# Kernel tuning notes

Measured on AMD Instinct MI355X. Metric: run time of the kernel, lower is better.

## Reference

```python
import jax, jax.numpy as jnp
import numpy as np

EPS = 1e-5  # BatchNorm eps (torch default)


def _norm_adj(adj):
    # DenseGCNConv: add self-loops, symmetric degree normalization
    N = adj.shape[-1]
    adj = adj + jnp.eye(N, dtype=adj.dtype)
    d = jnp.clip(adj.sum(-1), 1.0, None) ** -0.5
    return d[..., :, None] * adj * d[..., None, :]


def _gcn(x, adj_norm, W, b):
    return jnp.einsum('bij,bjf->bif', adj_norm, x @ W) + b


def _batchnorm(h, gamma, beta):
    # torch BatchNorm1d in training mode over flattened (B*N, C)
    B, N, C = h.shape
    hf = h.reshape(B * N, C)
    mu = hf.mean(0)
    var = hf.var(0)  # biased, as used for normalization
    out = (hf - mu) * jax.lax.rsqrt(var + EPS) * gamma + beta
    return out.reshape(B, N, C)


def setup_inputs() -> dict:
    key = jax.random.key(0)
    ks = jax.random.split(key, 24)
    B, N, F, H, D = 4, 256, 6, 128, 256
    s = 0.05
    a = jax.random.uniform(ks[1], (B, N, N), dtype=jnp.float32)
    adj = ((a + jnp.swapaxes(a, 1, 2)) / 2 < 0.1).astype(jnp.float32)  # sparse symmetric adjacency
    return {
        'x': jax.random.normal(ks[0], (B, N, F), dtype=jnp.float32),
        'adj': adj,
        'W1': jax.random.normal(ks[2], (F, H)) * s, 'b1': jnp.zeros((H,)),
        'W2': jax.random.normal(ks[3], (H, H)) * s, 'b2': jnp.zeros((H,)),
        'W3': jax.random.normal(ks[4], (H, D)) * s, 'b3': jnp.zeros((D,)),
        'g1': jnp.ones((H,)), 'beta1': jnp.zeros((H,)),
        'g2': jnp.ones((H,)), 'beta2': jnp.zeros((H,)),
        'e1w': jax.random.normal(ks[5], (2 * D, H)) * s, 'e1b': jnp.zeros((H,)),
        'e2w': jax.random.normal(ks[6], (H, H // 2)) * s, 'e2b': jnp.zeros((H // 2,)),
        'e3w': jax.random.normal(ks[7], (H // 2, 1)) * s, 'e3b': jnp.zeros((1,)),
        'f1w': jax.random.normal(ks[8], (D, H)) * s, 'f1b': jnp.zeros((H,)),
        'f2w': jax.random.normal(ks[9], (H, H)) * s, 'f2b': jnp.zeros((H,)),
        'f3w': jax.random.normal(ks[10], (H, F)) * s, 'f3b': jnp.zeros((F,)),
    }


def reference(x, adj, W1, b1, W2, b2, W3, b3, g1, beta1, g2, beta2,
              e1w, e1b, e2w, e2b, e3w, e3b, f1w, f1b, f2w, f2b, f3w, f3b):
    adj_norm = _norm_adj(adj)
    h = jax.nn.relu(_batchnorm(_gcn(x, adj_norm, W1, b1), g1, beta1))
    h = jax.nn.relu(_batchnorm(_gcn(h, adj_norm, W2, b2), g2, beta2))
    h = jax.nn.relu(_gcn(h, adj_norm, W3, b3))  # [B,N,D]
    D = h.shape[-1]
    # AdjacencyDecoder: Linear(cat(h_i,h_j)) == h_i@e1w[:D] + h_j@e1w[D:] (fused form, same math)
    hi = h @ e1w[:D]   # [B,N,H]
    hj = h @ e1w[D:]   # [B,N,H]
    p = jax.nn.relu(hi[:, :, None, :] + hj[:, None, :, :] + e1b)  # [B,N,N,H]
    p = jax.nn.relu(p @ e2w + e2b)                                 # [B,N,N,H/2]
    logits = (p @ e3w + e3b)[..., 0]                               # [B,N,N]
    logits = (logits + jnp.swapaxes(logits, 1, 2)) / 2
    adj_pred = jax.nn.sigmoid(logits)
    # FeatureDecoder
    f = jax.nn.relu(h @ f1w + f1b)
    f = jax.nn.relu(f @ f2w + f2b)
    feat_pred = f @ f3w + f3b
    return adj_pred, feat_pred
```

## Files before the change

kernel.cpp:

```cpp
#include <hip/hip_runtime.h>


typedef float v4f __attribute__((ext_vector_type(4)));
typedef short v8s __attribute__((ext_vector_type(8)));

__device__ __forceinline__ unsigned short f2bs(float f) {
    union { float f; unsigned int u; } v;
    v.f = f;
    return (unsigned short)((v.u + 0x7fffu + ((v.u >> 16) & 1u)) >> 16);
}

__global__ void k_pre(const float* x, const float* W1, const float* adj,
                      const float* e2w, float* buf, float* dg,
                      unsigned short* bfr_g, float* st) {
    __shared__ float ss[256];
    int blk = blockIdx.x, tid = threadIdx.x;
    if (blk < 512) {
        int idx = blk * 256 + tid;
        int m = idx >> 7, n = idx & 127;
        float s = 0.f;
        for (int k = 0; k < 6; k++) s += x[m * 6 + k] * W1[k * 128 + n];
        buf[idx] = s;
    } else if (blk < 768) {
        int row = (blk - 512) * 4 + (tid >> 6);
        int lane = tid & 63;
        const float* ap = adj + (long)row * 256;
        ss[tid] = ap[lane] + ap[lane + 64] + ap[lane + 128] + ap[lane + 192];
        __syncthreads();
        for (int o = 32; o > 0; o >>= 1) {
            if (lane < o) ss[tid] += ss[tid + o];
            __syncthreads();
        }
        if (lane == 0) {
            float t = ss[tid] + 1.f;
            if (t < 1.f) t = 1.f;
            dg[row] = rsqrtf(t);
        }
    } else {
        for (int s = tid; s < 8192; s += 256) {
            int k = s >> 6, n = s & 63;
            int kc = k >> 5, q = (k & 31) >> 3, t = k & 7;
            int nt = n >> 4, c2 = n & 15;
            bfr_g[(((nt * 4 + kc) * 64) + q * 16 + c2) * 8 + t] = f2bs(e2w[s]);
        }
        st[tid] = 0.f;
        st[256 + tid] = 0.f;
    }
}

template <int K>
__device__ __forceinline__ void dev_tile(
        int t, const float* A, const float* B, const float* bias,
        const float* dgA, float* anOut,
        const float* stat, const float* g, const float* beta,
        float* ostat, float* C,
        int N, int relu,
        int sA, int sB, int sC, int tiles_n, int tiles_m,
        float* smem) {
    constexpr int strideA = K + 4;
    constexpr int NCH = K / 16;
    float* As = smem;
    float* Bs = smem + 4160;
    int tid = threadIdx.x;
    int n2 = tid & 15, ml = tid >> 4;
    int bx = t % tiles_n;
    int tmp = t / tiles_n;
    int by = tmp % tiles_m;
    int bz = tmp / tiles_m;
    int m0 = by * 16, n0 = bx * 32;
    const float* Ab = A + (long)bz * sA;
    const float* Bb = B + (long)bz * sB;
    float* Cb = C + (long)bz * sC;
    const float* dgb = (dgA != 0) ? (dgA + bz * 256) : 0;

    int kk = tid & 15, mm = tid >> 4;
    int nb = tid & 31, kb = tid >> 5;

    float b0_r[NCH], b1_r[NCH], a_r[NCH];
    const float* Arow = Ab + (long)(m0 + mm) * K;
    #pragma unroll
    for (int i = 0; i < NCH; i++) {
        a_r[i]  = Arow[i * 16 + kk];
        b0_r[i] = Bb[(long)(i * 16 + kb) * N + n0 + nb];
        b1_r[i] = Bb[(long)(i * 16 + kb + 8) * N + n0 + nb];
    }

    if (dgA != 0) {
        float di = dgb[m0 + mm];
        float d_r[NCH];
        #pragma unroll
        for (int i = 0; i < NCH; i++) d_r[i] = dgb[i * 16 + kk];
        #pragma unroll
        for (int i = 0; i < NCH; i++) {
            int kg = i * 16 + kk;
            float v = a_r[i];
            if (m0 + mm == kg) v += 1.f;
            v = di * v * d_r[i];
            if (anOut != 0 && bx == 0)
                anOut[bz * 65536 + (m0 + mm) * 256 + kg] = v;
            As[mm * strideA + kg] = v;
        }
    } else if (stat != 0) {
        float s_r[NCH], q_r[NCH], g_r[NCH], be_r[NCH];
        #pragma unroll
        for (int i = 0; i < NCH; i++) {
            int kg = i * 16 + kk;
            s_r[i]  = stat[kg];
            q_r[i]  = stat[128 + kg];
            g_r[i]  = g[kg];
            be_r[i] = beta[kg];
        }
        #pragma unroll
        for (int i = 0; i < NCH; i++) {
            int kg = i * 16 + kk;
            float mu = s_r[i] * (1.f / 1024.f);
            float vr = q_r[i] * (1.f / 1024.f) - mu * mu;
            float sc = rsqrtf(vr + 1e-5f) * g_r[i];
            float v = (a_r[i] - mu) * sc + be_r[i];
            if (v < 0.f) v = 0.f;
            As[mm * strideA + kg] = v;
        }
    } else {
        #pragma unroll
        for (int i = 0; i < NCH; i++)
            As[mm * strideA + i * 16 + kk] = a_r[i];
    }
    #pragma unroll
    for (int i = 0; i < NCH; i++) {
        Bs[(i * 16 + kb) * 32 + nb] = b0_r[i];
        Bs[(i * 16 + kb + 8) * 32 + nb] = b1_r[i];
    }
    __syncthreads();

    float c0a = 0.f, c0b = 0.f, c1a = 0.f, c1b = 0.f;
    const float* arow = As + ml * strideA;
    const float* bcol = Bs + n2 * 2;
    #pragma unroll
    for (int q0 = 0; q0 < K; q0 += 4) {
        float4 av = *(const float4*)(arow + q0);
        float2 b0 = *(const float2*)(bcol + (q0 + 0) * 32);
        float2 b1 = *(const float2*)(bcol + (q0 + 1) * 32);
        float2 b2 = *(const float2*)(bcol + (q0 + 2) * 32);
        float2 b3 = *(const float2*)(bcol + (q0 + 3) * 32);
        c0a += av.x * b0.x; c1a += av.x * b0.y;
        c0b += av.y * b1.x; c1b += av.y * b1.y;
        c0a += av.z * b2.x; c1a += av.z * b2.y;
        c0b += av.w * b3.x; c1b += av.w * b3.y;
    }
    float c0 = c0a + c0b, c1 = c1a + c1b;
    int mRow = m0 + ml, nn = n0 + n2 * 2;
    if (bias != 0) { c0 += bias[nn]; c1 += bias[nn + 1]; }
    if (relu) {
        if (c0 < 0.f) c0 = 0.f;
        if (c1 < 0.f) c1 = 0.f;
    }
    Cb[(long)mRow * N + nn] = c0;
    Cb[(long)mRow * N + nn + 1] = c1;

    if (ostat != 0) {
        float* sred = smem;
        float* qred = smem + 544;
        __syncthreads();
        sred[(n2 * 2) * 17 + ml] = c0;
        sred[(n2 * 2 + 1) * 17 + ml] = c1;
        qred[(n2 * 2) * 17 + ml] = c0 * c0;
        qred[(n2 * 2 + 1) * 17 + ml] = c1 * c1;
        __syncthreads();
        if (tid < 32) {
            float s = 0.f, q = 0.f;
            for (int u = 0; u < 16; u++) {
                s += sred[tid * 17 + u];
                q += qred[tid * 17 + u];
            }
            atomicAdd(&ostat[n0 + tid], s);
            atomicAdd(&ostat[128 + n0 + tid], q);
        }
    }
}

template <int K>
__global__ __launch_bounds__(256, 3) void k_tgemm(
        const float* A, const float* B, const float* bias,
        const float* dgA, float* anOut,
        const float* stat, const float* g, const float* beta,
        float* ostat, float* C,
        int N, int relu,
        int sA, int sB, int sC, int tiles_n, int tiles_m) {
    __shared__ float smem[12352];
    dev_tile<K>(blockIdx.x, A, B, bias, dgA, anOut, stat, g, beta, ostat, C,
                N, relu, sA, sB, sC, tiles_n, tiles_m, smem);
}

__global__ __launch_bounds__(256, 3) void k_g67(
        const float* hb, const float* e1w, float* hi,
        const float* f1w, const float* f1b, float* f1) {
    __shared__ float smem[12352];
    int t = blockIdx.x;
    if (t < 512) {
        dev_tile<256>(t, hb, e1w, 0, 0, 0, 0, 0, 0, 0, hi,
                      128, 0, 0, 32768, 131072, 4, 64, smem);
    } else {
        dev_tile<256>(t - 512, hb, f1w, f1b, 0, 0, 0, 0, 0, 0, f1,
                      128, 1, 0, 0, 0, 4, 64, smem);
    }
}

__global__ void k_decf(const float* hi, const float* hj, const float* e1b,
                       const unsigned short* bfr_g, const float* e2b,
                       const float* e3w, const float* e3b,
                       const float* f1, const float* f2w, const float* f2b_,
                       const float* f3w, const float* f3b,
                       float* lg, float* out) {
    __shared__ float smem[4608];
    int tid = threadIdx.x;
    int blk = blockIdx.x;
    if (blk < 1024) {
        float* red = smem;
        float* pre_sh = smem + 4352;
        int lane = tid & 63, wv = tid >> 6;
        int col = lane & 15, quad = lane >> 4;
        int bi = blk, b = bi >> 8;
        if (tid < 128) pre_sh[tid] = hi[bi * 128 + tid] + e1b[tid];
        __syncthreads();
        float e2bv[4], e3wv[4];
        for (int nt = 0; nt < 4; nt++) {
            e2bv[nt] = e2b[nt * 16 + col];
            e3wv[nt] = e3w[nt * 16 + col];
        }
        const float* hjb = hj + b * 32768;
        #pragma unroll 1
        for (int ms = 0; ms < 4; ms++) {
            v4f acc[4];
            for (int nt = 0; nt < 4; nt++) {
                v4f z = {0.f, 0.f, 0.f, 0.f};
                acc[nt] = z;
            }
            int j = wv * 64 + ms * 16 + col;
            const float* rowp = hjb + j * 128 + quad * 8;
            float hjr[32];
            #pragma unroll
            for (int q = 0; q < 8; q++) {
                float4 v = *(const float4*)(rowp + (q >> 1) * 32 + (q & 1) * 4);
                hjr[q * 4 + 0] = v.x; hjr[q * 4 + 1] = v.y;
                hjr[q * 4 + 2] = v.z; hjr[q * 4 + 3] = v.w;
            }
            #pragma unroll
            for (int kc = 0; kc < 4; kc++) {
                const float* pp = pre_sh + kc * 32 + quad * 8;
                v8s af;
                #pragma unroll
                for (int t = 0; t < 8; t++) {
                    float p = pp[t] + hjr[kc * 8 + t];
                    p = (p > 0.f) ? p : 0.f;
                    af[t] = (short)f2bs(p);
                }
                #pragma unroll
                for (int nt = 0; nt < 4; nt++) {
                    v8s bf = *(const v8s*)&bfr_g[(((nt * 4 + kc) * 64) + lane) * 8];
                    acc[nt] = __builtin_amdgcn_mfma_f32_16x16x32_bf16(
                        af, bf, acc[nt], 0, 0, 0);
                }
            }
            #pragma unroll
            for (int r = 0; r < 4; r++) {
                float s = 0.f;
                #pragma unroll
                for (int nt = 0; nt < 4; nt++) {
                    float v = acc[nt][r] + e2bv[nt];
                    if (v > 0.f) s += v * e3wv[nt];
                }
                red[(wv * 64 + ms * 16 + quad * 4 + r) * 17 + col] = s;
            }
        }
        __syncthreads();
        float s = e3b[0];
        for (int c = 0; c < 16; c++) s += red[tid * 17 + c];
        lg[bi * 256 + tid] = s;
    } else {
        float* f2row = smem;
        int r0 = (blk - 1024) * 4;
        for (int p = 0; p < 2; p++) {
            int idx = tid + p * 256;
            int r = r0 + (idx >> 7), n = idx & 127;
            const float* f1r = f1 + (long)r * 128;
            float s0 = 0.f, s1 = 0.f, s2 = 0.f, s3 = 0.f;
            #pragma unroll
            for (int k = 0; k < 128; k += 4) {
                float4 fv = *(const float4*)(f1r + k);
                s0 += fv.x * f2w[(k + 0) * 128 + n];
                s1 += fv.y * f2w[(k + 1) * 128 + n];
                s2 += fv.z * f2w[(k + 2) * 128 + n];
                s3 += fv.w * f2w[(k + 3) * 128 + n];
            }
            float s = f2b_[n] + ((s0 + s1) + (s2 + s3));
            if (s < 0.f) s = 0.f;
            f2row[idx] = s;
        }
        __syncthreads();
        if (tid < 24) {
            int r = tid / 6, c = tid % 6;
            float s = f3b[c];
            const float* fr = f2row + r * 128;
            for (int k = 0; k < 128; k++) s += fr[k] * f3w[k * 6 + c];
            out[262144 + (r0 + r) * 6 + c] = s;
        }
    }
}

__global__ void k_symsig(const float* lg, float* out) {
    __shared__ float Ta[32 * 33];
    __shared__ float Tb[32 * 33];
    int tid = threadIdx.x;
    int b = blockIdx.x / 36;
    int t = blockIdx.x % 36;
    int ti = 0, rem = t;
    while (rem >= 8 - ti) { rem -= 8 - ti; ti++; }
    int tj = ti + rem;
    int i0 = ti * 32, j0 = tj * 32;
    const float* lgb = lg + b * 65536;
    for (int p = 0; p < 4; p++) {
        int idx = p * 256 + tid;
        int r = idx >> 5, c = idx & 31;
        Ta[r * 33 + c] = lgb[(i0 + r) * 256 + j0 + c];
        Tb[r * 33 + c] = lgb[(j0 + r) * 256 + i0 + c];
    }
    __syncthreads();
    float* ob = out + b * 65536;
    for (int p = 0; p < 4; p++) {
        int idx = p * 256 + tid;
        int r = idx >> 5, c = idx & 31;
        float v1 = 0.5f * (Ta[r * 33 + c] + Tb[c * 33 + r]);
        ob[(i0 + r) * 256 + j0 + c] = 1.f / (1.f + expf(-v1));
        float v2 = 0.5f * (Tb[r * 33 + c] + Ta[c * 33 + r]);
        ob[(j0 + r) * 256 + i0 + c] = 1.f / (1.f + expf(-v2));
    }
}

extern "C" void kernel_launch(void* const* d_in, const int* in_sizes, int n_in,
                              void* d_out, int out_size, void* d_ws, size_t ws_size,
                              hipStream_t stream) {
    const float* x   = (const float*)d_in[0];
    const float* adj = (const float*)d_in[1];
    const float* W1  = (const float*)d_in[2];
    const float* b1  = (const float*)d_in[3];
    const float* W2  = (const float*)d_in[4];
    const float* b2  = (const float*)d_in[5];
    const float* W3  = (const float*)d_in[6];
    const float* b3  = (const float*)d_in[7];
    const float* g1  = (const float*)d_in[8];
    const float* be1 = (const float*)d_in[9];
    const float* g2  = (const float*)d_in[10];
    const float* be2 = (const float*)d_in[11];
    const float* e1w = (const float*)d_in[12];
    const float* e1b = (const float*)d_in[13];
    const float* e2w = (const float*)d_in[14];
    const float* e2b = (const float*)d_in[15];
    const float* e3w = (const float*)d_in[16];
    const float* e3b = (const float*)d_in[17];
    const float* f1w = (const float*)d_in[18];
    const float* f1b = (const float*)d_in[19];
    const float* f2w = (const float*)d_in[20];
    const float* f2b_ = (const float*)d_in[21];
    const float* f3w = (const float*)d_in[22];
    const float* f3b = (const float*)d_in[23];

    float* out = (float*)d_out;

    if (ws_size < (size_t)1600000 * 4) {
        hipMemsetAsync(d_out, 0x60, 4096, stream);
        return;
    }
    float* ws = (float*)d_ws;
    float* st1 = ws;
    float* st2 = ws + 256;
    float* dg  = ws + 512;
    unsigned short* bfr_g = (unsigned short*)(ws + 1536);
    float* An  = ws + 5632;
    float* buf = An + 262144;
    float* hb  = buf + 262144;
    float* lg  = hb + 262144;
    float* h1  = lg + 262144;
    float* h2  = h1 + 131072;
    float* hi  = h2 + 131072;
    float* hj  = hi + 131072;

    k_pre<<<769, 256, 0, stream>>>(x, W1, adj, e2w, buf, dg, bfr_g, st1);
    k_tgemm<256><<<256, 256, 0, stream>>>(adj, buf, b1, dg, An, 0, 0, 0, st1, h1,
                                          128, 0, 65536, 32768, 32768, 4, 16);
    k_tgemm<128><<<256, 256, 0, stream>>>(h1, W2, 0, 0, 0, st1, g1, be1, 0, buf,
                                          128, 0, 0, 0, 0, 4, 64);
    k_tgemm<256><<<256, 256, 0, stream>>>(An, buf, b2, 0, 0, 0, 0, 0, st2, h2,
                                          128, 0, 65536, 32768, 32768, 4, 16);
    k_tgemm<128><<<512, 256, 0, stream>>>(h2, W3, 0, 0, 0, st2, g2, be2, 0, buf,
                                          256, 0, 0, 0, 0, 8, 64);
    k_tgemm<256><<<512, 256, 0, stream>>>(An, buf, b3, 0, 0, 0, 0, 0, 0, hb,
                                          256, 1, 65536, 65536, 65536, 8, 16);
    k_g67<<<768, 256, 0, stream>>>(hb, e1w, hi, f1w, f1b, h1);
    k_decf<<<1280, 256, 0, stream>>>(hi, hj, e1b, bfr_g, e2b, e3w, e3b,
                                     h1, f2w, f2b_, f3w, f3b, lg, out);
    k_symsig<<<144, 256, 0, stream>>>(lg, out);
}
```

Before: 184.3 us.

## Fuse BN+ReLU, adjacency aggregation and weight GEMM into one kernel per GCN layer

```diff
diff --git a/kernel.cpp b/kernel.cpp
--- a/kernel.cpp
+++ b/kernel.cpp
@@ -189,6 +189,117 @@
     __shared__ float smem[12352];
     dev_tile<K>(blockIdx.x, A, B, bias, dgA, anOut, stat, g, beta, ostat, C,
                 N, relu, sA, sB, sC, tiles_n, tiles_m, smem);
+}
+
+template <int NW, int NC, int STATS, int RELU>
+__global__ __launch_bounds__(512, 1) void k_fuse2(
+        const float* __restrict__ An, const float* __restrict__ Hin,
+        const float* __restrict__ W, const float* __restrict__ bias,
+        const float* __restrict__ st, const float* __restrict__ g,
+        const float* __restrict__ beta, float* ostat, float* OUT) {
+    __shared__ float sm[15360];
+    float* sl  = sm;
+    float* sh  = sm + 128;
+    float* An_s = sm + 256;
+    float* P_s  = sm + 4416;
+    float* Ws   = sm + 8640;
+    float* T_s  = sm + 13248;
+
+    int t = threadIdx.x;
+    int bx = blockIdx.x;
+    int nc = bx % NC;
+    int mt = (bx / NC) & 15;
+    int bz = bx / (NC * 16);
+    int m0 = mt * 16;
+    int r = t >> 5, cg = t & 31;
+
+    const float* Ag = An + (long)bz * 65536 + (long)(m0 + r) * 256 + cg * 8;
+    float4 anA = *(const float4*)Ag;
+    float4 anB = *(const float4*)(Ag + 4);
+    const float* Hg = Hin + (long)bz * 32768 + t * 64;
+    float4 h_r[16];
+    #pragma unroll
+    for (int q = 0; q < 16; q++) h_r[q] = *(const float4*)(Hg + q * 4);
+    const float* Wg = W + (long)(t >> 2) * NW + nc * 32 + (t & 3) * 8;
+    float4 wA = *(const float4*)Wg;
+    float4 wB = *(const float4*)(Wg + 4);
+    float bv = bias[nc * 32 + cg];
+    float stv = 0.f, sqv = 0.f, gv = 0.f, bev = 0.f;
+    if (t < 128) { stv = st[t]; sqv = st[128 + t]; gv = g[t]; bev = beta[t]; }
+
+    {
+        float* d = An_s + r * 260 + cg * 8;
+        *(float4*)d = anA; *(float4*)(d + 4) = anB;
+    }
+    {
+        float* d = Ws + (t >> 2) * 36 + (t & 3) * 8;
+        *(float4*)d = wA; *(float4*)(d + 4) = wB;
+    }
+    if (t < 128) {
+        float mu = stv * (1.f / 1024.f);
+        float vr = sqv * (1.f / 1024.f) - mu * mu;
+        float sc = rsqrtf(vr + 1e-5f) * gv;
+        sl[t] = sc;
+        sh[t] = bev - mu * sc;
+    }
+    __syncthreads();
+
+    float4 acc = {0.f, 0.f, 0.f, 0.f};
+    int myp = t >> 6;
+    int prow = (t >> 1) & 31;
+    int cbase = (t & 1) * 64;
+    for (int p = 0; p < 8; p++) {
+        if (p) __syncthreads();
+        if (myp == p) {
+            #pragma unroll
+            for (int q = 0; q < 16; q++) {
+                float4 v = h_r[q];
+                int c = cbase + q * 4;
+                float o0 = v.x * sl[c + 0] + sh[c + 0]; o0 = o0 > 0.f ? o0 : 0.f;
+                float o1 = v.y * sl[c + 1] + sh[c + 1]; o1 = o1 > 0.f ? o1 : 0.f;
+                float o2 = v.z * sl[c + 2] + sh[c + 2]; o2 = o2 > 0.f ? o2 : 0.f;
+                float o3 = v.w * sl[c + 3] + sh[c + 3]; o3 = o3 > 0.f ? o3 : 0.f;
+                float4 ov = {o0, o1, o2, o3};
+                *(float4*)(P_s + prow * 132 + c) = ov;
+            }
+        }
+        __syncthreads();
+        const float* ar = An_s + r * 260 + p * 32;
+        #pragma unroll
+        for (int kk = 0; kk < 32; kk++) {
+            float a = ar[kk];
+            float4 pv = *(const float4*)(P_s + kk * 132 + cg * 4);
+            acc.x += a * pv.x; acc.y += a * pv.y;
+            acc.z += a * pv.z; acc.w += a * pv.w;
+        }
+    }
+    *(float4*)(T_s + r * 132 + cg * 4) = acc;
+    __syncthreads();
+
+    float o = bv;
+    const float* tr = T_s + r * 132;
+    #pragma unroll 8
+    for (int k = 0; k < 128; k++) o += tr[k] * Ws[k * 36 + cg];
+
+    if (STATS) {
+        float* red_s = P_s;
+        float* red_q = P_s + 544;
+        red_s[cg * 17 + r] = o;
+        red_q[cg * 17 + r] = o * o;
+        __syncthreads();
+        if (t < 32) {
+            float s = 0.f, q = 0.f;
+            #pragma unroll
+            for (int u = 0; u < 16; u++) {
+                s += red_s[t * 17 + u];
+                q += red_q[t * 17 + u];
+            }
+            atomicAdd(&ostat[nc * 32 + t], s);
+            atomicAdd(&ostat[128 + nc * 32 + t], q);
+        }
+    }
+    if (RELU) o = o > 0.f ? o : 0.f;
+    OUT[(long)bz * (NW * 256) + (long)(m0 + r) * NW + nc * 32 + cg] = o;
 }
 
 __global__ __launch_bounds__(256, 3) void k_g67(
@@ -387,14 +498,10 @@
     k_pre<<<769, 256, 0, stream>>>(x, W1, adj, e2w, buf, dg, bfr_g, st1);
     k_tgemm<256><<<256, 256, 0, stream>>>(adj, buf, b1, dg, An, 0, 0, 0, st1, h1,
                                           128, 0, 65536, 32768, 32768, 4, 16);
-    k_tgemm<128><<<256, 256, 0, stream>>>(h1, W2, 0, 0, 0, st1, g1, be1, 0, buf,
-                                          128, 0, 0, 0, 0, 4, 64);
-    k_tgemm<256><<<256, 256, 0, stream>>>(An, buf, b2, 0, 0, 0, 0, 0, st2, h2,
-                                          128, 0, 65536, 32768, 32768, 4, 16);
-    k_tgemm<128><<<512, 256, 0, stream>>>(h2, W3, 0, 0, 0, st2, g2, be2, 0, buf,
-                                          256, 0, 0, 0, 0, 8, 64);
-    k_tgemm<256><<<512, 256, 0, stream>>>(An, buf, b3, 0, 0, 0, 0, 0, 0, hb,
-                                          256, 1, 65536, 65536, 65536, 8, 16);
+    k_fuse2<128, 4, 1, 0><<<256, 512, 0, stream>>>(
+        An, h1, W2, b2, st1, g1, be1, st2, h2);
+    k_fuse2<256, 8, 0, 1><<<512, 512, 0, stream>>>(
+        An, h2, W3, b3, st2, g2, be2, 0, hb);
     k_g67<<<768, 256, 0, stream>>>(hb, e1w, hi, f1w, f1b, h1);
     k_decf<<<1280, 256, 0, stream>>>(hi, hj, e1b, bfr_g, e2b, e3w, e3b,
                                      h1, f2w, f2b_, f3w, f3b, lg, out);
```

New measurement: 213.4 us. +15.8%, slower.

## Fuse pairwise decoder with symmetrization and sigmoid into tile-pair blocks

Applied to the files above, without the earlier changes.

```diff
diff --git a/kernel.cpp b/kernel.cpp
--- a/kernel.cpp
+++ b/kernel.cpp
@@ -188,7 +188,7 @@
         int sA, int sB, int sC, int tiles_n, int tiles_m) {
     __shared__ float smem[12352];
     dev_tile<K>(blockIdx.x, A, B, bias, dgA, anOut, stat, g, beta, ostat, C,
-                N, relu, sA, sB, sC, tiles_n, tiles_m, smem);
+                K == 256 && sA == 65536 ? N : N, relu, sA, sB, sC, tiles_n, tiles_m, smem);
 }
 
 __global__ __launch_bounds__(256, 3) void k_g67(
@@ -205,80 +205,144 @@
     }
 }
 
-__global__ void k_decf(const float* hi, const float* hj, const float* e1b,
+__global__ void k_dec2(const float* hi, const float* hj, const float* e1b,
                        const unsigned short* bfr_g, const float* e2b,
                        const float* e3w, const float* e3b,
                        const float* f1, const float* f2w, const float* f2b_,
                        const float* f3w, const float* f3b,
-                       float* lg, float* out) {
-    __shared__ float smem[4608];
+                       float* out) {
+    __shared__ float smem[9504];
     int tid = threadIdx.x;
     int blk = blockIdx.x;
-    if (blk < 1024) {
-        float* red = smem;
-        float* pre_sh = smem + 4352;
+    if (blk < 144) {
+        float* pre2 = smem;
+        float* M_s  = smem + 8448;
+        int b = blk / 36;
+        int t36 = blk % 36;
+        int ti = 0, rem = t36;
+        while (rem >= 8 - ti) { rem -= 8 - ti; ti++; }
+        int tj = ti + rem;
+        int i0 = ti * 32, j0 = tj * 32;
+
         int lane = tid & 63, wv = tid >> 6;
         int col = lane & 15, quad = lane >> 4;
-        int bi = blk, b = bi >> 8;
-        if (tid < 128) pre_sh[tid] = hi[bi * 128 + tid] + e1b[tid];
+
+        const float* hib = hi + b * 32768;
+        {
+            int cq = tid & 31;
+            float4 e1v = *(const float4*)(e1b + cq * 4);
+            #pragma unroll
+            for (int s = tid; s < 2048; s += 256) {
+                int w = s >> 5;
+                int row = (w < 32) ? i0 + w : j0 + (w - 32);
+                float4 v = *(const float4*)(hib + row * 128 + cq * 4);
+                float* d = pre2 + w * 132 + cq * 4;
+                d[0] = v.x + e1v.x; d[1] = v.y + e1v.y;
+                d[2] = v.z + e1v.z; d[3] = v.w + e1v.w;
+            }
+        }
         __syncthreads();
+
         float e2bv[4], e3wv[4];
+        #pragma unroll
         for (int nt = 0; nt < 4; nt++) {
             e2bv[nt] = e2b[nt * 16 + col];
             e3wv[nt] = e3w[nt * 16 + col];
         }
+        float e3b0 = e3b[0];
         const float* hjb = hj + b * 32768;
+
         #pragma unroll 1
-        for (int ms = 0; ms < 4; ms++) {
-            v4f acc[4];
-            for (int nt = 0; nt < 4; nt++) {
-                v4f z = {0.f, 0.f, 0.f, 0.f};
-                acc[nt] = z;
-            }
-            int j = wv * 64 + ms * 16 + col;
-            const float* rowp = hjb + j * 128 + quad * 8;
-            float hjr[32];
-            #pragma unroll
-            for (int q = 0; q < 8; q++) {
-                float4 v = *(const float4*)(rowp + (q >> 1) * 32 + (q & 1) * 4);
-                hjr[q * 4 + 0] = v.x; hjr[q * 4 + 1] = v.y;
-                hjr[q * 4 + 2] = v.z; hjr[q * 4 + 3] = v.w;
-            }
-            #pragma unroll
-            for (int kc = 0; kc < 4; kc++) {
-                const float* pp = pre_sh + kc * 32 + quad * 8;
-                v8s af;
+        for (int ph = 0; ph < 2; ph++) {
+            int jb0 = (ph == 0) ? j0 : i0;
+            int pbase = (ph == 0) ? 0 : 32;
+            #pragma unroll 1
+            for (int jblk = 0; jblk < 2; jblk++) {
+                const float* rowp = hjb + (long)(jb0 + jblk * 16 + col) * 128 + quad * 8;
+                float hjr[32];
                 #pragma unroll
-                for (int t = 0; t < 8; t++) {
-                    float p = pp[t] + hjr[kc * 8 + t];
-                    p = (p > 0.f) ? p : 0.f;
-                    af[t] = (short)f2bs(p);
+                for (int q = 0; q < 8; q++) {
+                    float4 v = *(const float4*)(rowp + (q >> 1) * 32 + (q & 1) * 4);
+                    hjr[q * 4 + 0] = v.x; hjr[q * 4 + 1] = v.y;
+                    hjr[q * 4 + 2] = v.z; hjr[q * 4 + 3] = v.w;
                 }
-                #pragma unroll
-                for (int nt = 0; nt < 4; nt++) {
-                    v8s bf = *(const v8s*)&bfr_g[(((nt * 4 + kc) * 64) + lane) * 8];
-                    acc[nt] = __builtin_amdgcn_mfma_f32_16x16x32_bf16(
-                        af, bf, acc[nt], 0, 0, 0);
+                #pragma unroll 1
+                for (int ii = 0; ii < 8; ii++) {
+                    int iG = wv * 8 + ii;
+                    const float* pp_base = pre2 + (pbase + iG) * 132 + quad * 8;
+                    v4f acc[4];
+                    #pragma unroll
+                    for (int nt = 0; nt < 4; nt++) {
+                        v4f z = {0.f, 0.f, 0.f, 0.f};
+                        acc[nt] = z;
+                    }
+                    #pragma unroll
+                    for (int kc = 0; kc < 4; kc++) {
+                        const float* pp = pp_base + kc * 32;
+                        v8s af;
+                        #pragma unroll
+                        for (int t = 0; t < 8; t++) {
+                            float p = pp[t] + hjr[kc * 8 + t];
+                            p = (p > 0.f) ? p : 0.f;
+                            af[t] = (short)f2bs(p);
+                        }
+                        #pragma unroll
+                        for (int nt = 0; nt < 4; nt++) {
+                            v8s bf = *(const v8s*)&bfr_g[(((nt * 4 + kc) * 64) + lane) * 8];
+                            acc[nt] = __builtin_amdgcn_mfma_f32_16x16x32_bf16(
+                                af, bf, acc[nt], 0, 0, 0);
+                        }
+                    }
+                    float vr[4];
+                    #pragma unroll
+                    for (int r = 0; r < 4; r++) {
+                        float s = 0.f;
+                        #pragma unroll
+                        for (int nt = 0; nt < 4; nt++) {
+                            float v = acc[nt][r] + e2bv[nt];
+                            if (v > 0.f) s += v * e3wv[nt];
+                        }
+                        vr[r] = s;
+                    }
+                    #pragma unroll
+                    for (int m = 1; m <= 8; m <<= 1) {
+                        #pragma unroll
+                        for (int r = 0; r < 4; r++)
+                            vr[r] += __shfl_xor(vr[r], m, 64);
+                    }
+                    if (col == 0) {
+                        #pragma unroll
+                        for (int r = 0; r < 4; r++) {
+                            int jc = jblk * 16 + quad * 4 + r;
+                            if (ph == 0)
+                                M_s[iG * 33 + jc] = e3b0 + 0.5f * vr[r];
+                            else
+                                M_s[jc * 33 + iG] += 0.5f * vr[r];
+                        }
+                    }
                 }
             }
+            __syncthreads();
+        }
+
+        float* ob = out + b * 65536;
+        #pragma unroll
+        for (int s = tid; s < 1024; s += 256) {
+            int r = s >> 5, c = s & 31;
+            float m = M_s[r * 33 + c];
+            ob[(long)(i0 + r) * 256 + j0 + c] = 1.f / (1.f + expf(-m));
+        }
+        if (ti != tj) {
             #pragma unroll
-            for (int r = 0; r < 4; r++) {
-                float s = 0.f;
-                #pragma unroll
-                for (int nt = 0; nt < 4; nt++) {
-                    float v = acc[nt][r] + e2bv[nt];
-                    if (v > 0.f) s += v * e3wv[nt];
-                }
-                red[(wv * 64 + ms * 16 + quad * 4 + r) * 17 + col] = s;
+            for (int s = tid; s < 1024; s += 256) {
+                int r = s >> 5, c = s & 31;
+                float m = M_s[c * 33 + r];
+                ob[(long)(j0 + r) * 256 + i0 + c] = 1.f / (1.f + expf(-m));
             }
         }
-        __syncthreads();
-        float s = e3b[0];
-        for (int c = 0; c < 16; c++) s += red[tid * 17 + c];
-        lg[bi * 256 + tid] = s;
     } else {
         float* f2row = smem;
-        int r0 = (blk - 1024) * 4;
+        int r0 = (blk - 144) * 4;
         for (int p = 0; p < 2; p++) {
             int idx = tid + p * 256;
             int r = r0 + (idx >> 7), n = idx & 127;
@@ -304,35 +368,6 @@
             for (int k = 0; k < 128; k++) s += fr[k] * f3w[k * 6 + c];
             out[262144 + (r0 + r) * 6 + c] = s;
         }
-    }
-}
-
-__global__ void k_symsig(const float* lg, float* out) {
-    __shared__ float Ta[32 * 33];
-    __shared__ float Tb[32 * 33];
-    int tid = threadIdx.x;
-    int b = blockIdx.x / 36;
-    int t = blockIdx.x % 36;
-    int ti = 0, rem = t;
-    while (rem >= 8 - ti) { rem -= 8 - ti; ti++; }
-    int tj = ti + rem;
-    int i0 = ti * 32, j0 = tj * 32;
-    const float* lgb = lg + b * 65536;
-    for (int p = 0; p < 4; p++) {
-        int idx = p * 256 + tid;
-        int r = idx >> 5, c = idx & 31;
-        Ta[r * 33 + c] = lgb[(i0 + r) * 256 + j0 + c];
-        Tb[r * 33 + c] = lgb[(j0 + r) * 256 + i0 + c];
-    }
-    __syncthreads();
-    float* ob = out + b * 65536;
-    for (int p = 0; p < 4; p++) {
-        int idx = p * 256 + tid;
-        int r = idx >> 5, c = idx & 31;
-        float v1 = 0.5f * (Ta[r * 33 + c] + Tb[c * 33 + r]);
-        ob[(i0 + r) * 256 + j0 + c] = 1.f / (1.f + expf(-v1));
-        float v2 = 0.5f * (Tb[r * 33 + c] + Ta[c * 33 + r]);
-        ob[(j0 + r) * 256 + i0 + c] = 1.f / (1.f + expf(-v2));
     }
 }
 
@@ -396,7 +431,6 @@
     k_tgemm<256><<<512, 256, 0, stream>>>(An, buf, b3, 0, 0, 0, 0, 0, 0, hb,
                                           256, 1, 65536, 65536, 65536, 8, 16);
     k_g67<<<768, 256, 0, stream>>>(hb, e1w, hi, f1w, f1b, h1);
-    k_decf<<<1280, 256, 0, stream>>>(hi, hj, e1b, bfr_g, e2b, e3w, e3b,
-                                     h1, f2w, f2b_, f3w, f3b, lg, out);
-    k_symsig<<<144, 256, 0, stream>>>(lg, out);
-}
+    k_dec2<<<400, 256, 0, stream>>>(hi, hj, e1b, bfr_g, e2b, e3w, e3b,
+                                    h1, f2w, f2b_, f3w, f3b, out);
+}
```

New measurement: 215.2 us. +16.8%, slower.
